# Performance work log

Measured on AMD Instinct MI355X. Metric: run time of the kernel, lower is better.

Reference implementation:

```python
import jax, jax.numpy as jnp
import numpy as np

B, N, F = 2, 2048, 64
H, C = 4, 32          # attention heads, channels per head
HID = 128             # hidden_size
HIN = H * C           # hidden_size_in = 128
MASK = -10e9          # spektral dense-GAT mask constant


def setup_inputs() -> dict:
    key = jax.random.key(0)
    ks = jax.random.split(key, 48)
    inp = {}
    inp['x'] = jax.random.normal(ks[0], (B, N, F), dtype=jnp.float32)
    adj = (jax.random.uniform(ks[1], (B, N, N)) < 0.03).astype(jnp.float32)
    inp['a'] = jnp.clip(adj + jnp.eye(N, dtype=jnp.float32)[None], 0.0, 1.0)
    inp['h_p'] = jax.random.normal(ks[2], (B, N, HID), dtype=jnp.float32) * 0.1
    inp['h_mu'] = jax.random.normal(ks[3], (B, N, HID), dtype=jnp.float32) * 0.1
    inp['h_sigma'] = jax.random.normal(ks[4], (B, N, HID), dtype=jnp.float32) * 0.1
    # GAT params
    inp['gat_kernel'] = jax.random.normal(ks[5], (F, H, C), dtype=jnp.float32) / np.float32(np.sqrt(F))
    inp['gat_attn_self'] = jax.random.normal(ks[6], (H, C), dtype=jnp.float32) * 0.1
    inp['gat_attn_neigh'] = jax.random.normal(ks[7], (H, C), dtype=jnp.float32) * 0.1
    inp['gat_bias'] = jnp.zeros((H * C,), dtype=jnp.float32)
    # GRU-style gate params for p / mu / sigma
    ki = 8
    for nm in ('p', 'mu', 'sigma'):
        for g in ('u', 'r', 'c'):
            inp[f'W_{g}_{nm}'] = jax.random.normal(ks[ki], (HID + HIN, HID), dtype=jnp.float32) / np.float32(np.sqrt(HID + HIN)); ki += 1
            inp[f'b_{g}_{nm}'] = jax.random.normal(ks[ki], (N, 1), dtype=jnp.float32) * 0.05; ki += 1
    # bilinear decoders
    for nm in ('p', 'mu', 'sigma'):
        inp[f'R_{nm}'] = jax.random.normal(ks[ki], (HID, HID), dtype=jnp.float32) / np.float32(np.sqrt(HID)); ki += 1
    return inp


def _gat(x, a, kernel, attn_self, attn_neigh, bias):
    # dense spektral GATConv, concat_heads=True, no activation
    h = jnp.einsum('bnf,fhc->bnhc', x, kernel)                 # [B,N,H,C]
    s_self = jnp.einsum('bnhc,hc->bnh', h, attn_self)          # [B,N,H]
    s_neigh = jnp.einsum('bnhc,hc->bnh', h, attn_neigh)        # [B,N,H]
    scores = s_self[:, :, None, :] + s_neigh[:, None, :, :]    # [B,N,N,H]
    scores = jax.nn.leaky_relu(scores, negative_slope=0.2)
    scores = scores + MASK * (1.0 - a)[..., None]
    attn = jax.nn.softmax(scores, axis=2)                      # softmax over neighbors j
    out = jnp.einsum('bijh,bjhc->bihc', attn, h)               # [B,N,H,C]
    return out.reshape(out.shape[0], out.shape[1], H * C) + bias


def _gru(conv, h, Wu, Wr, Wc, bu, br, bc):
    ch = jnp.concatenate([conv, h], axis=-1)                   # [B,N,HIN+HID]
    u = jax.nn.sigmoid(bu + ch @ Wu)                           # bias [N,1] broadcasts
    r = jax.nn.sigmoid(br + ch @ Wr)
    c = jnp.tanh(bc + jnp.concatenate([conv, r * h], axis=-1) @ Wc)
    return u * h + (1.0 - u) * c


def _bilinear(h, R):
    return jnp.einsum('bnh,hk,bmk->bnm', h, R, h)              # x R x^T


def reference(x, a, h_p, h_mu, h_sigma,
              gat_kernel, gat_attn_self, gat_attn_neigh, gat_bias,
              W_u_p, b_u_p, W_r_p, b_r_p, W_c_p, b_c_p,
              W_u_mu, b_u_mu, W_r_mu, b_r_mu, W_c_mu, b_c_mu,
              W_u_sigma, b_u_sigma, W_r_sigma, b_r_sigma, W_c_sigma, b_c_sigma,
              R_p, R_mu, R_sigma):
    conv = _gat(x, a, gat_kernel, gat_attn_self, gat_attn_neigh, gat_bias)
    hp = _gru(conv, h_p, W_u_p, W_r_p, W_c_p, b_u_p, b_r_p, b_c_p)
    hmu = _gru(conv, h_mu, W_u_mu, W_r_mu, W_c_mu, b_u_mu, b_r_mu, b_c_mu)
    hsg = _gru(conv, h_sigma, W_u_sigma, W_r_sigma, W_c_sigma, b_u_sigma, b_r_sigma, b_c_sigma)
    p = _bilinear(hp, R_p)
    mu = _bilinear(hmu, R_mu)
    sigma = _bilinear(hsg, R_sigma)
    logits = jnp.stack([p, mu, sigma], axis=-1)                # [B,N,N,3]
    return logits, hp, hmu, hsg
```

## Files before the change

kernel.cpp:

```cpp
#include <hip/hip_runtime.h>
#include <hip/hip_bf16.h>

typedef __attribute__((ext_vector_type(4))) float f32x4;
typedef __attribute__((ext_vector_type(8))) short bf16x8;

static constexpr int B   = 2;
static constexpr int N   = 2048;
static constexpr int F   = 64;
static constexpr int H   = 4;
static constexpr int HID = 128;
static constexpr int BN  = B * N;
static constexpr size_t LOG_SZ = (size_t)B * N * N * 3;

__device__ __forceinline__ float sigmoidf_(float x) { return 1.0f / (1.0f + __expf(-x)); }
__device__ __forceinline__ float tanhf_(float x) {
  float e = __expf(2.0f * x);
  return 1.0f - 2.0f / (e + 1.0f);
}
__device__ __forceinline__ void split_bf16(float v, short& hi, short& lo) {
  unsigned u = __float_as_uint(v);
  unsigned hr = (u + 0x7FFFu + ((u >> 16) & 1u)) >> 16;
  hi = (short)hr;
  float hv = __uint_as_float(hr << 16);
  float res = v - hv;
  unsigned u2 = __float_as_uint(res);
  lo = (short)((u2 + 0x7FFFu + ((u2 >> 16) & 1u)) >> 16);
}

__device__ __forceinline__ void stage16(const short* gp, short* lp) {
  __builtin_amdgcn_global_load_lds(
      (const __attribute__((address_space(1))) void*)gp,
      (__attribute__((address_space(3))) void*)lp, 16, 0, 0);
}

struct PreArgs {
  const float* x; const float* gk; const float* asel; const float* anei;
  float* hfeat; float* sself; float* sneigh;
  const float* h[3];
  short* hh[3]; short* hl[3];
  const float* src[12];
  short* whi[12]; short* wlo[12];
  int nks[12];
};
__global__ __launch_bounds__(256) void k_pre(PreArgs pa) {
  const int bid = blockIdx.x;
  if (bid < BN / 2) {
    const int t = threadIdx.x;
    const int r = t >> 7, tt = t & 127;
    const int bn = bid * 2 + r;
    __shared__ float xs[2][F];
    if (tt < F) xs[r][tt] = pa.x[(size_t)bn * F + tt];
    const size_t o = (size_t)bn * HID + tt;
    { short hi, lo; split_bf16(pa.h[0][o], hi, lo); pa.hh[0][o] = hi; pa.hl[0][o] = lo; }
    { short hi, lo; split_bf16(pa.h[1][o], hi, lo); pa.hh[1][o] = hi; pa.hl[1][o] = lo; }
    { short hi, lo; split_bf16(pa.h[2][o], hi, lo); pa.hh[2][o] = hi; pa.hl[2][o] = lo; }
    __syncthreads();
    float acc = 0.f;
    #pragma unroll 8
    for (int f = 0; f < F; ++f) acc += xs[r][f] * pa.gk[f * HID + tt];
    pa.hfeat[o] = acc;
    float ps = acc * pa.asel[tt];
    float pn = acc * pa.anei[tt];
    #pragma unroll
    for (int d = 16; d >= 1; d >>= 1) {
      ps += __shfl_xor(ps, d, 32);
      pn += __shfl_xor(pn, d, 32);
    }
    if ((tt & 31) == 0) {
      pa.sself [bn * H + (tt >> 5)] = ps;
      pa.sneigh[bn * H + (tt >> 5)] = pn;
    }
  } else {
    const int pb = bid - BN / 2;
    const int m = pb >> 3, cf = pb & 7;
    const int nksv = pa.nks[m];
    const int wv = threadIdx.x >> 6, lane = threadIdx.x & 63;
    const float* src = pa.src[m];
    short* ph = pa.whi[m];
    short* pl = pa.wlo[m];
    const int col = cf * 16 + (lane & 15);
    const int krow = (lane >> 4) * 8;
    for (int ks = wv; ks < nksv; ks += 4) {
      bf16x8 vh, vl;
      #pragma unroll
      for (int e = 0; e < 8; ++e) {
        const int k = ks * 32 + krow + e;
        short hi, lo; split_bf16(src[(size_t)k * HID + col], hi, lo);
        vh[e] = hi; vl[e] = lo;
      }
      const size_t o = (((size_t)cf * nksv + ks) * 64 + lane) * 8;
      *(bf16x8*)&ph[o] = vh;
      *(bf16x8*)&pl[o] = vl;
    }
  }
}

__global__ __launch_bounds__(256) void k_attn(
    const float* __restrict__ a, const float* __restrict__ hfeat,
    const float* __restrict__ sself, const float* __restrict__ sneigh,
    const float* __restrict__ bias,
    short* __restrict__ conv_hi, short* __restrict__ conv_lo) {
  const int wv   = threadIdx.x >> 6;
  const int lane = threadIdx.x & 63;
  const int bi   = blockIdx.x;
  const int bbase = bi & ~(N - 1);
  __shared__ int   nbr[4][128];
  __shared__ float wts[4][128][4];
  __shared__ float racc[4][128];
  __shared__ float rden[4][4];
  int*   nb      = nbr[wv];
  float (*wt)[4] = wts[wv];

  const float si0 = sself[bi * H + 0];
  const float si1 = sself[bi * H + 1];
  const float si2 = sself[bi * H + 2];
  const float si3 = sself[bi * H + 3];
  float den0 = 0.f, den1 = 0.f, den2 = 0.f, den3 = 0.f;
  float acc0 = 0.f, acc1 = 0.f;
  const unsigned long long lmlt = ((unsigned long long)1 << lane) - 1ull;
  const float* arow = a + (size_t)bi * N + wv * 512;
  const float* hb   = hfeat + (size_t)bbase * HID;
  const float* snb  = sneigh + (size_t)bbase * H;
  const int h0 = lane >> 5;
  const int jbase0 = wv * 512;
  int num = 0;

  auto flush = [&]() {
    asm volatile("s_waitcnt lgkmcnt(0)" ::: "memory");
    for (int n = lane; n < num; n += 64) {
      const int j = nb[n];
      f32x4 sn = *(const f32x4*)&snb[(size_t)j * H];
      float s0 = si0 + sn[0]; s0 = (s0 > 0.f) ? s0 : 0.2f * s0;
      float s1 = si1 + sn[1]; s1 = (s1 > 0.f) ? s1 : 0.2f * s1;
      float s2 = si2 + sn[2]; s2 = (s2 > 0.f) ? s2 : 0.2f * s2;
      float s3 = si3 + sn[3]; s3 = (s3 > 0.f) ? s3 : 0.2f * s3;
      float w0 = __expf(s0), w1 = __expf(s1), w2 = __expf(s2), w3 = __expf(s3);
      wt[n][0] = w0; wt[n][1] = w1; wt[n][2] = w2; wt[n][3] = w3;
      den0 += w0; den1 += w1; den2 += w2; den3 += w3;
    }
    asm volatile("s_waitcnt lgkmcnt(0)" ::: "memory");
    #pragma unroll 4
    for (int n = 0; n < num; ++n) {
      const int j  = nb[n];
      const float wA = wt[n][h0];
      const float wB = wt[n][h0 + 2];
      const float* hr = hb + (size_t)j * HID;
      acc0 += wA * hr[lane];
      acc1 += wB * hr[lane + 64];
    }
    asm volatile("s_waitcnt lgkmcnt(0)" ::: "memory");
    num = 0;
  };

  #pragma unroll
  for (int jb = 0; jb < 512; jb += 256) {
    f32x4 av = *(const f32x4*)&arow[jb + lane * 4];
    #pragma unroll
    for (int e = 0; e < 4; ++e) {
      const unsigned long long m = __ballot(av[e] > 0.5f);
      if (av[e] > 0.5f) {
        const int pos = num + __popcll(m & lmlt);
        nb[pos] = jbase0 + jb + lane * 4 + e;
      }
      num += __popcll(m);
      if (num > 64) flush();
    }
  }
  if (num > 0) flush();

  #pragma unroll
  for (int d = 32; d >= 1; d >>= 1) {
    den0 += __shfl_xor(den0, d, 64);
    den1 += __shfl_xor(den1, d, 64);
    den2 += __shfl_xor(den2, d, 64);
    den3 += __shfl_xor(den3, d, 64);
  }
  racc[wv][lane]      = acc0;
  racc[wv][lane + 64] = acc1;
  if (lane == 0) {
    rden[wv][0] = den0; rden[wv][1] = den1;
    rden[wv][2] = den2; rden[wv][3] = den3;
  }
  __syncthreads();
  if (threadIdx.x < HID) {
    const int ch = threadIdx.x;
    const float tot = racc[0][ch] + racc[1][ch] + racc[2][ch] + racc[3][ch];
    const int hh = ch >> 5;
    const float dd = rden[0][hh] + rden[1][hh] + rden[2][hh] + rden[3][hh];
    const float v = tot / dd + bias[ch];
    short hi, lo; split_bf16(v, hi, lo);
    conv_hi[(size_t)bi * HID + ch] = hi;
    conv_lo[(size_t)bi * HID + ch] = lo;
  }
}

struct GArgs {
  const short* chi; const short* clo;
  const float* h[3];
  const short* hhi[3]; const short* hlo[3];
  const float* bu[3]; const float* br[3]; const float* bc[3];
  const short* WuH[3]; const short* WuL[3];
  const short* WrH[3]; const short* WrL[3];
  const short* WcH[3]; const short* WcL[3];
  const short* RtH[3]; const short* RtL[3];
  float* u_ws[3];
  short* rhh[3]; short* rhl[3];
  short* hph[3]; short* hpl[3];
  float* hout[3]; __hip_bfloat16* hb[3]; __hip_bfloat16* gb[3];
};

__global__ __launch_bounds__(256) void k_ur(GArgs ga) {
  const int wv = threadIdx.x >> 6, lane = threadIdx.x & 63;
  const int bx = blockIdx.x, cg = blockIdx.y;
  const int gate = blockIdx.z & 1, cell = blockIdx.z >> 1;
  const int lr = lane & 15, lg = lane >> 4, kb = lg * 8;
  const int R0 = bx * 64 + wv * 16;
  __shared__ short wlds[2][16][64][8];

  bf16x8 a_h[8], a_l[8];
  {
    const size_t ab = (size_t)(R0 + lr) * HID + kb;
    const short* hhi = ga.hhi[cell]; const short* hlo = ga.hlo[cell];
    #pragma unroll
    for (int ks = 0; ks < 4; ++ks) {
      a_h[ks]     = *(const bf16x8*)&ga.chi[ab + ks * 32];
      a_l[ks]     = *(const bf16x8*)&ga.clo[ab + ks * 32];
      a_h[4 + ks] = *(const bf16x8*)&hhi[ab + ks * 32];
      a_l[4 + ks] = *(const bf16x8*)&hlo[ab + ks * 32];
    }
  }
  {
    const short* WH = gate ? ga.WrH[cell] : ga.WuH[cell];
    const short* WL = gate ? ga.WrL[cell] : ga.WuL[cell];
    #pragma unroll
    for (int i = 0; i < 8; ++i) {
      const int fid = wv * 8 + i;
      const int combo = fid >> 4, f = fid & 15;
      const short* src = combo ? WL : WH;
      const short* gp = src + (((size_t)((cg * 2 + (f >> 3)) * 8 + (f & 7))) * 64 + lane) * 8;
      stage16(gp, &wlds[combo][f][0][0]);
    }
  }
  asm volatile("s_waitcnt vmcnt(0)" ::: "memory");
  __syncthreads();

  f32x4 acc[2] = {};
  #pragma unroll
  for (int ks = 0; ks < 8; ++ks) {
    const bf16x8 ah = a_h[ks], al = a_l[ks];
    #pragma unroll
    for (int cfl = 0; cfl < 2; ++cfl) {
      const int f = cfl * 8 + ks;
      bf16x8 bh = *(const bf16x8*)&wlds[0][f][lane][0];
      bf16x8 bl = *(const bf16x8*)&wlds[1][f][lane][0];
      acc[cfl] = __builtin_amdgcn_mfma_f32_16x16x32_bf16(ah, bh, acc[cfl], 0, 0, 0);
      acc[cfl] = __builtin_amdgcn_mfma_f32_16x16x32_bf16(ah, bl, acc[cfl], 0, 0, 0);
      acc[cfl] = __builtin_amdgcn_mfma_f32_16x16x32_bf16(al, bh, acc[cfl], 0, 0, 0);
    }
  }
  if (gate == 0) {
    const float* bu = ga.bu[cell];
    float* uws = ga.u_ws[cell];
    #pragma unroll
    for (int cfl = 0; cfl < 2; ++cfl) {
      const int col = cg * 32 + cfl * 16 + lr;
      #pragma unroll
      for (int q = 0; q < 4; ++q) {
        const int row = R0 + lg * 4 + q;
        uws[(size_t)row * HID + col] = sigmoidf_(acc[cfl][q] + bu[row & (N - 1)]);
      }
    }
  } else {
    const float* br = ga.br[cell];
    const float* hsrc = ga.h[cell];
    short* rhh = ga.rhh[cell]; short* rhl = ga.rhl[cell];
    #pragma unroll
    for (int cfl = 0; cfl < 2; ++cfl) {
      const int col = cg * 32 + cfl * 16 + lr;
      #pragma unroll
      for (int q = 0; q < 4; ++q) {
        const int row = R0 + lg * 4 + q;
        const float rv = sigmoidf_(acc[cfl][q] + br[row & (N - 1)]);
        const float rhv = rv * hsrc[(size_t)row * HID + col];
        short hi, lo; split_bf16(rhv, hi, lo);
        rhh[(size_t)row * HID + col] = hi;
        rhl[(size_t)row * HID + col] = lo;
      }
    }
  }
}

__global__ __launch_bounds__(256) void k_c(GArgs ga) {
  const int wv = threadIdx.x >> 6, lane = threadIdx.x & 63;
  const int bx = blockIdx.x, cg = blockIdx.y, cell = blockIdx.z;
  const int lr = lane & 15, lg = lane >> 4, kb = lg * 8;
  const int R0 = bx * 64 + wv * 16;
  __shared__ short wlds[2][16][64][8];

  bf16x8 a_h[8], a_l[8];
  {
    const size_t ab = (size_t)(R0 + lr) * HID + kb;
    const short* rhh = ga.rhh[cell]; const short* rhl = ga.rhl[cell];
    #pragma unroll
    for (int ks = 0; ks < 4; ++ks) {
      a_h[ks]     = *(const bf16x8*)&ga.chi[ab + ks * 32];
      a_l[ks]     = *(const bf16x8*)&ga.clo[ab + ks * 32];
      a_h[4 + ks] = *(const bf16x8*)&rhh[ab + ks * 32];
      a_l[4 + ks] = *(const bf16x8*)&rhl[ab + ks * 32];
    }
  }
  {
    const short* WH = ga.WcH[cell];
    const short* WL = ga.WcL[cell];
    #pragma unroll
    for (int i = 0; i < 8; ++i) {
      const int fid = wv * 8 + i;
      const int combo = fid >> 4, f = fid & 15;
      const short* src = combo ? WL : WH;
      const short* gp = src + (((size_t)((cg * 2 + (f >> 3)) * 8 + (f & 7))) * 64 + lane) * 8;
      stage16(gp, &wlds[combo][f][0][0]);
    }
  }
  asm volatile("s_waitcnt vmcnt(0)" ::: "memory");
  __syncthreads();

  f32x4 acc[2] = {};
  #pragma unroll
  for (int ks = 0; ks < 8; ++ks) {
    const bf16x8 ah = a_h[ks], al = a_l[ks];
    #pragma unroll
    for (int cfl = 0; cfl < 2; ++cfl) {
      const int f = cfl * 8 + ks;
      bf16x8 bh = *(const bf16x8*)&wlds[0][f][lane][0];
      bf16x8 bl = *(const bf16x8*)&wlds[1][f][lane][0];
      acc[cfl] = __builtin_amdgcn_mfma_f32_16x16x32_bf16(ah, bh, acc[cfl], 0, 0, 0);
      acc[cfl] = __builtin_amdgcn_mfma_f32_16x16x32_bf16(ah, bl, acc[cfl], 0, 0, 0);
      acc[cfl] = __builtin_amdgcn_mfma_f32_16x16x32_bf16(al, bh, acc[cfl], 0, 0, 0);
    }
  }
  const float* bc = ga.bc[cell];
  const float* uw = ga.u_ws[cell];
  const float* hsrc = ga.h[cell];
  float* hout = ga.hout[cell];
  __hip_bfloat16* hbo = ga.hb[cell];
  short* hph = ga.hph[cell]; short* hpl = ga.hpl[cell];
  #pragma unroll
  for (int cfl = 0; cfl < 2; ++cfl) {
    const int col = cg * 32 + cfl * 16 + lr;
    #pragma unroll
    for (int q = 0; q < 4; ++q) {
      const int row = R0 + lg * 4 + q;
      const float cv = tanhf_(acc[cfl][q] + bc[row & (N - 1)]);
      const float uv = uw[(size_t)row * HID + col];
      const float hv = hsrc[(size_t)row * HID + col];
      const float o = uv * hv + (1.f - uv) * cv;
      __builtin_nontemporal_store(o, &hout[(size_t)row * HID + col]);
      hbo[(size_t)row * HID + col] = __float2bfloat16(o);
      short hi, lo; split_bf16(o, hi, lo);
      hph[(size_t)row * HID + col] = hi;
      hpl[(size_t)row * HID + col] = lo;
    }
  }
}

__global__ __launch_bounds__(256) void k_g(GArgs ga) {
  const int wv = threadIdx.x >> 6, lane = threadIdx.x & 63;
  const int bx = blockIdx.x, cg = blockIdx.y, cell = blockIdx.z;
  const int lr = lane & 15, lg = lane >> 4, kb = lg * 8;
  const int R0 = bx * 64 + wv * 16;
  __shared__ short wlds[2][8][64][8];

  bf16x8 a_h[4], a_l[4];
  {
    const size_t ab = (size_t)(R0 + lr) * HID + kb;
    const short* hph = ga.hph[cell]; const short* hpl = ga.hpl[cell];
    #pragma unroll
    for (int ks = 0; ks < 4; ++ks) {
      a_h[ks] = *(const bf16x8*)&hph[ab + ks * 32];
      a_l[ks] = *(const bf16x8*)&hpl[ab + ks * 32];
    }
  }
  {
    #pragma unroll
    for (int i = 0; i < 4; ++i) {
      const int fid = wv * 4 + i;
      const int combo = fid >> 3, f = fid & 7;
      const short* src = combo ? ga.RtL[cell] : ga.RtH[cell];
      const short* gp = src + (((size_t)((cg * 2 + (f >> 2)) * 4 + (f & 3))) * 64 + lane) * 8;
      stage16(gp, &wlds[combo][f][0][0]);
    }
  }
  asm volatile("s_waitcnt vmcnt(0)" ::: "memory");
  __syncthreads();

  f32x4 acc[2] = {};
  #pragma unroll
  for (int ks = 0; ks < 4; ++ks) {
    const bf16x8 ah = a_h[ks], al = a_l[ks];
    #pragma unroll
    for (int cfl = 0; cfl < 2; ++cfl) {
      const int f = cfl * 4 + ks;
      bf16x8 bh = *(const bf16x8*)&wlds[0][f][lane][0];
      bf16x8 bl = *(const bf16x8*)&wlds[1][f][lane][0];
      acc[cfl] = __builtin_amdgcn_mfma_f32_16x16x32_bf16(ah, bh, acc[cfl], 0, 0, 0);
      acc[cfl] = __builtin_amdgcn_mfma_f32_16x16x32_bf16(ah, bl, acc[cfl], 0, 0, 0);
      acc[cfl] = __builtin_amdgcn_mfma_f32_16x16x32_bf16(al, bh, acc[cfl], 0, 0, 0);
    }
  }
  __hip_bfloat16* gbo = ga.gb[cell];
  #pragma unroll
  for (int cfl = 0; cfl < 2; ++cfl) {
    const int col = cg * 32 + cfl * 16 + lr;
    #pragma unroll
    for (int q = 0; q < 4; ++q) {
      const int row = R0 + lg * 4 + q;
      gbo[(size_t)row * HID + col] = __float2bfloat16(acc[cfl][q]);
    }
  }
}

__global__ __launch_bounds__(256) void k_bilinear(
    const __hip_bfloat16* __restrict__ g0, const __hip_bfloat16* __restrict__ g1,
    const __hip_bfloat16* __restrict__ g2, const __hip_bfloat16* __restrict__ h0,
    const __hip_bfloat16* __restrict__ h1, const __hip_bfloat16* __restrict__ h2,
    float* __restrict__ out) {
  const int ti = blockIdx.x, tj = blockIdx.y, b = blockIdx.z;
  const int t = threadIdx.x;
  const int w = t >> 6, l = t & 63;
  const int wi = w >> 1, wj = w & 1;
  const int i_base = ti * 64 + wi * 32;
  const int j_base = tj * 64 + wj * 32;
  const __hip_bfloat16* gbs[3] = {g0, g1, g2};
  const __hip_bfloat16* hbs[3] = {h0, h1, h2};
  const int lr = l & 15;
  const int kb = (l >> 4) * 8;
  f32x4 acc[3][2][2] = {};
  for (int k0 = 0; k0 < HID; k0 += 32) {
    bf16x8 af[3][2], bfr[3][2];
    #pragma unroll
    for (int d = 0; d < 3; ++d) {
      #pragma unroll
      for (int m = 0; m < 2; ++m) {
        af[d][m]  = *(const bf16x8*)&gbs[d][(size_t)(b * N + i_base + m * 16 + lr) * HID + k0 + kb];
        bfr[d][m] = *(const bf16x8*)&hbs[d][(size_t)(b * N + j_base + m * 16 + lr) * HID + k0 + kb];
      }
    }
    #pragma unroll
    for (int d = 0; d < 3; ++d)
      #pragma unroll
      for (int mi = 0; mi < 2; ++mi)
        #pragma unroll
        for (int mj = 0; mj < 2; ++mj)
          acc[d][mi][mj] = __builtin_amdgcn_mfma_f32_16x16x32_bf16(
              af[d][mi], bfr[d][mj], acc[d][mi][mj], 0, 0, 0);
  }
  const int orow = (l >> 4) * 4;
  const int col  = l & 15;
  #pragma unroll
  for (int mi = 0; mi < 2; ++mi)
    #pragma unroll
    for (int mj = 0; mj < 2; ++mj)
      #pragma unroll
      for (int r = 0; r < 4; ++r) {
        const int row = i_base + mi * 16 + orow + r;
        const int cc  = j_base + mj * 16 + col;
        float* p = &out[(((size_t)(b * N + row)) * N + cc) * 3];
        __builtin_nontemporal_store(acc[0][mi][mj][r], p + 0);
        __builtin_nontemporal_store(acc[1][mi][mj][r], p + 1);
        __builtin_nontemporal_store(acc[2][mi][mj][r], p + 2);
      }
}

extern "C" void kernel_launch(void* const* d_in, const int* in_sizes, int n_in,
                              void* d_out, int out_size, void* d_ws, size_t ws_size,
                              hipStream_t stream) {
  (void)in_sizes; (void)n_in; (void)out_size; (void)ws_size;
  const float* a    = (const float*)d_in[1];
  const float* bias = (const float*)d_in[8];

  float* ws      = (float*)d_ws;
  float* hfeat   = ws;
  float* sself   = hfeat + (size_t)BN * HID;
  float* sneigh  = sself + (size_t)BN * H;
  float* u_ws0   = sneigh + (size_t)BN * H;
  short* sp      = (short*)(u_ws0 + 3 * (size_t)BN * HID);
  auto alloc_s = [&](size_t n) { short* p = sp; sp += n; return p; };

  short* conv_hi = alloc_s((size_t)BN * HID);
  short* conv_lo = alloc_s((size_t)BN * HID);
  short* h_hi[3]; short* h_lo[3];
  for (int c = 0; c < 3; ++c) { h_hi[c] = alloc_s((size_t)BN * HID); h_lo[c] = alloc_s((size_t)BN * HID); }
  short* rh_hi[3]; short* rh_lo[3];
  for (int c = 0; c < 3; ++c) { rh_hi[c] = alloc_s((size_t)BN * HID); rh_lo[c] = alloc_s((size_t)BN * HID); }
  short* hp_hi[3]; short* hp_lo[3];
  for (int c = 0; c < 3; ++c) { hp_hi[c] = alloc_s((size_t)BN * HID); hp_lo[c] = alloc_s((size_t)BN * HID); }
  __hip_bfloat16* hbb[3]; __hip_bfloat16* gbb[3];
  for (int c = 0; c < 3; ++c) {
    hbb[c] = (__hip_bfloat16*)alloc_s((size_t)BN * HID);
    gbb[c] = (__hip_bfloat16*)alloc_s((size_t)BN * HID);
  }

  float* out = (float*)d_out;

  PreArgs pa;
  pa.x = (const float*)d_in[0];
  pa.gk = (const float*)d_in[5];
  pa.asel = (const float*)d_in[6];
  pa.anei = (const float*)d_in[7];
  pa.hfeat = hfeat; pa.sself = sself; pa.sneigh = sneigh;

  GArgs ga;
  ga.chi = conv_hi; ga.clo = conv_lo;
  ga.h[0] = (const float*)d_in[2];
  ga.h[1] = (const float*)d_in[3];
  ga.h[2] = (const float*)d_in[4];
  for (int c = 0; c < 3; ++c) {
    pa.h[c] = ga.h[c];
    pa.hh[c] = h_hi[c]; pa.hl[c] = h_lo[c];
    const int base = 9 + c * 6;
    ga.hhi[c] = h_hi[c]; ga.hlo[c] = h_lo[c];
    ga.bu[c] = (const float*)d_in[base + 1];
    ga.br[c] = (const float*)d_in[base + 3];
    ga.bc[c] = (const float*)d_in[base + 5];
    short* wu_h = alloc_s(256 * 128); short* wu_l = alloc_s(256 * 128);
    short* wr_h = alloc_s(256 * 128); short* wr_l = alloc_s(256 * 128);
    short* wc_h = alloc_s(256 * 128); short* wc_l = alloc_s(256 * 128);
    short* rt_h = alloc_s(128 * 128); short* rt_l = alloc_s(128 * 128);
    const int pb = c * 4;
    pa.src[pb + 0] = (const float*)d_in[base + 0]; pa.whi[pb + 0] = wu_h; pa.wlo[pb + 0] = wu_l; pa.nks[pb + 0] = 8;
    pa.src[pb + 1] = (const float*)d_in[base + 2]; pa.whi[pb + 1] = wr_h; pa.wlo[pb + 1] = wr_l; pa.nks[pb + 1] = 8;
    pa.src[pb + 2] = (const float*)d_in[base + 4]; pa.whi[pb + 2] = wc_h; pa.wlo[pb + 2] = wc_l; pa.nks[pb + 2] = 8;
    pa.src[pb + 3] = (const float*)d_in[27 + c];   pa.whi[pb + 3] = rt_h; pa.wlo[pb + 3] = rt_l; pa.nks[pb + 3] = 4;
    ga.WuH[c] = wu_h; ga.WuL[c] = wu_l;
    ga.WrH[c] = wr_h; ga.WrL[c] = wr_l;
    ga.WcH[c] = wc_h; ga.WcL[c] = wc_l;
    ga.RtH[c] = rt_h; ga.RtL[c] = rt_l;
    ga.u_ws[c] = u_ws0 + (size_t)c * BN * HID;
    ga.rhh[c] = rh_hi[c]; ga.rhl[c] = rh_lo[c];
    ga.hph[c] = hp_hi[c]; ga.hpl[c] = hp_lo[c];
    ga.hout[c] = out + LOG_SZ + (size_t)c * BN * HID;
    ga.hb[c] = hbb[c];
    ga.gb[c] = gbb[c];
  }

  k_pre<<<BN / 2 + 96, 256, 0, stream>>>(pa);
  k_attn<<<BN, 256, 0, stream>>>(a, hfeat, sself, sneigh, bias, conv_hi, conv_lo);
  k_ur<<<dim3(BN / 64, 4, 6), 256, 0, stream>>>(ga);
  k_c<<<dim3(BN / 64, 4, 3), 256, 0, stream>>>(ga);
  k_g<<<dim3(BN / 64, 4, 3), 256, 0, stream>>>(ga);
  dim3 g2(N / 64, N / 64, B);
  k_bilinear<<<g2, 256, 0, stream>>>(gbb[0], gbb[1], gbb[2],
                                     hbb[0], hbb[1], hbb[2], out);
}
```

Baseline: 115.3 us.

## Fuse update and reset gates in one kernel; enlarge bilinear tiles with swizzled order

The u and r gate GEMMs now run in the same block, so the A-operand fragments (conv and h, hi/lo splits) are loaded once and reused for both gates, and the grid z-dimension halves. The bilinear kernel moves to 512-thread blocks covering 128 rows of the output tile and remaps block ids with a grouped swizzle to improve L2 reuse of the g/h operands. In exchange, k_ur uses twice the LDS and more accumulator registers, and there are fewer blocks in flight.

```diff
diff --git a/kernel.cpp b/kernel.cpp
--- a/kernel.cpp
+++ b/kernel.cpp
@@ -211,11 +211,10 @@
 
 __global__ __launch_bounds__(256) void k_ur(GArgs ga) {
   const int wv = threadIdx.x >> 6, lane = threadIdx.x & 63;
-  const int bx = blockIdx.x, cg = blockIdx.y;
-  const int gate = blockIdx.z & 1, cell = blockIdx.z >> 1;
+  const int bx = blockIdx.x, cg = blockIdx.y, cell = blockIdx.z;
   const int lr = lane & 15, lg = lane >> 4, kb = lg * 8;
   const int R0 = bx * 64 + wv * 16;
-  __shared__ short wlds[2][16][64][8];
+  __shared__ short wlds[4][16][64][8];
 
   bf16x8 a_h[8], a_l[8];
   {
@@ -230,62 +229,54 @@
     }
   }
   {
-    const short* WH = gate ? ga.WrH[cell] : ga.WuH[cell];
-    const short* WL = gate ? ga.WrL[cell] : ga.WuL[cell];
-    #pragma unroll
-    for (int i = 0; i < 8; ++i) {
-      const int fid = wv * 8 + i;
-      const int combo = fid >> 4, f = fid & 15;
-      const short* src = combo ? WL : WH;
-      const short* gp = src + (((size_t)((cg * 2 + (f >> 3)) * 8 + (f & 7))) * 64 + lane) * 8;
-      stage16(gp, &wlds[combo][f][0][0]);
+    const short* srcs[4] = { ga.WuH[cell], ga.WuL[cell], ga.WrH[cell], ga.WrL[cell] };
+    const short* sp = srcs[wv];
+    #pragma unroll
+    for (int f = 0; f < 16; ++f) {
+      const short* gp = sp + (((size_t)((cg * 2 + (f >> 3)) * 8 + (f & 7))) * 64 + lane) * 8;
+      stage16(gp, &wlds[wv][f][0][0]);
     }
   }
   asm volatile("s_waitcnt vmcnt(0)" ::: "memory");
   __syncthreads();
 
-  f32x4 acc[2] = {};
+  f32x4 au[2] = {}, ar[2] = {};
   #pragma unroll
   for (int ks = 0; ks < 8; ++ks) {
     const bf16x8 ah = a_h[ks], al = a_l[ks];
     #pragma unroll
     for (int cfl = 0; cfl < 2; ++cfl) {
       const int f = cfl * 8 + ks;
-      bf16x8 bh = *(const bf16x8*)&wlds[0][f][lane][0];
-      bf16x8 bl = *(const bf16x8*)&wlds[1][f][lane][0];
-      acc[cfl] = __builtin_amdgcn_mfma_f32_16x16x32_bf16(ah, bh, acc[cfl], 0, 0, 0);
-      acc[cfl] = __builtin_amdgcn_mfma_f32_16x16x32_bf16(ah, bl, acc[cfl], 0, 0, 0);
-      acc[cfl] = __builtin_amdgcn_mfma_f32_16x16x32_bf16(al, bh, acc[cfl], 0, 0, 0);
-    }
-  }
-  if (gate == 0) {
-    const float* bu = ga.bu[cell];
-    float* uws = ga.u_ws[cell];
-    #pragma unroll
-    for (int cfl = 0; cfl < 2; ++cfl) {
-      const int col = cg * 32 + cfl * 16 + lr;
-      #pragma unroll
-      for (int q = 0; q < 4; ++q) {
-        const int row = R0 + lg * 4 + q;
-        uws[(size_t)row * HID + col] = sigmoidf_(acc[cfl][q] + bu[row & (N - 1)]);
-      }
-    }
-  } else {
-    const float* br = ga.br[cell];
-    const float* hsrc = ga.h[cell];
-    short* rhh = ga.rhh[cell]; short* rhl = ga.rhl[cell];
-    #pragma unroll
-    for (int cfl = 0; cfl < 2; ++cfl) {
-      const int col = cg * 32 + cfl * 16 + lr;
-      #pragma unroll
-      for (int q = 0; q < 4; ++q) {
-        const int row = R0 + lg * 4 + q;
-        const float rv = sigmoidf_(acc[cfl][q] + br[row & (N - 1)]);
-        const float rhv = rv * hsrc[(size_t)row * HID + col];
-        short hi, lo; split_bf16(rhv, hi, lo);
-        rhh[(size_t)row * HID + col] = hi;
-        rhl[(size_t)row * HID + col] = lo;
-      }
+      bf16x8 buh = *(const bf16x8*)&wlds[0][f][lane][0];
+      bf16x8 bul = *(const bf16x8*)&wlds[1][f][lane][0];
+      bf16x8 brh = *(const bf16x8*)&wlds[2][f][lane][0];
+      bf16x8 brl = *(const bf16x8*)&wlds[3][f][lane][0];
+      au[cfl] = __builtin_amdgcn_mfma_f32_16x16x32_bf16(ah, buh, au[cfl], 0, 0, 0);
+      au[cfl] = __builtin_amdgcn_mfma_f32_16x16x32_bf16(ah, bul, au[cfl], 0, 0, 0);
+      au[cfl] = __builtin_amdgcn_mfma_f32_16x16x32_bf16(al, buh, au[cfl], 0, 0, 0);
+      ar[cfl] = __builtin_amdgcn_mfma_f32_16x16x32_bf16(ah, brh, ar[cfl], 0, 0, 0);
+      ar[cfl] = __builtin_amdgcn_mfma_f32_16x16x32_bf16(ah, brl, ar[cfl], 0, 0, 0);
+      ar[cfl] = __builtin_amdgcn_mfma_f32_16x16x32_bf16(al, brh, ar[cfl], 0, 0, 0);
+    }
+  }
+  const float* bu = ga.bu[cell];
+  const float* br = ga.br[cell];
+  const float* hsrc = ga.h[cell];
+  float* uws = ga.u_ws[cell];
+  short* rhh = ga.rhh[cell]; short* rhl = ga.rhl[cell];
+  #pragma unroll
+  for (int cfl = 0; cfl < 2; ++cfl) {
+    const int col = cg * 32 + cfl * 16 + lr;
+    #pragma unroll
+    for (int q = 0; q < 4; ++q) {
+      const int row = R0 + lg * 4 + q;
+      const int n = row & (N - 1);
+      uws[(size_t)row * HID + col] = sigmoidf_(au[cfl][q] + bu[n]);
+      const float rv = sigmoidf_(ar[cfl][q] + br[n]);
+      const float rhv = rv * hsrc[(size_t)row * HID + col];
+      short hi, lo; split_bf16(rhv, hi, lo);
+      rhh[(size_t)row * HID + col] = hi;
+      rhl[(size_t)row * HID + col] = lo;
     }
   }
 }
@@ -419,16 +410,19 @@
   }
 }
 
-__global__ __launch_bounds__(256) void k_bilinear(
+__global__ __launch_bounds__(512) void k_bilinear(
     const __hip_bfloat16* __restrict__ g0, const __hip_bfloat16* __restrict__ g1,
     const __hip_bfloat16* __restrict__ g2, const __hip_bfloat16* __restrict__ h0,
     const __hip_bfloat16* __restrict__ h1, const __hip_bfloat16* __restrict__ h2,
     float* __restrict__ out) {
-  const int ti = blockIdx.x, tj = blockIdx.y, b = blockIdx.z;
+  const int id  = blockIdx.y * 16 + blockIdx.x;
+  const int id2 = (id & 7) * 64 + (id >> 3);
+  const int ti = id2 & 15, tj = id2 >> 4;
+  const int b = blockIdx.z;
   const int t = threadIdx.x;
   const int w = t >> 6, l = t & 63;
   const int wi = w >> 1, wj = w & 1;
-  const int i_base = ti * 64 + wi * 32;
+  const int i_base = ti * 128 + wi * 32;
   const int j_base = tj * 64 + wj * 32;
   const __hip_bfloat16* gbs[3] = {g0, g1, g2};
   const __hip_bfloat16* hbs[3] = {h0, h1, h2};
@@ -545,10 +539,10 @@
 
   k_pre<<<BN / 2 + 96, 256, 0, stream>>>(pa);
   k_attn<<<BN, 256, 0, stream>>>(a, hfeat, sself, sneigh, bias, conv_hi, conv_lo);
-  k_ur<<<dim3(BN / 64, 4, 6), 256, 0, stream>>>(ga);
+  k_ur<<<dim3(BN / 64, 4, 3), 256, 0, stream>>>(ga);
   k_c<<<dim3(BN / 64, 4, 3), 256, 0, stream>>>(ga);
   k_g<<<dim3(BN / 64, 4, 3), 256, 0, stream>>>(ga);
-  dim3 g2(N / 64, N / 64, B);
-  k_bilinear<<<g2, 256, 0, stream>>>(gbb[0], gbb[1], gbb[2],
+  dim3 g2(N / 128, N / 64, B);
+  k_bilinear<<<g2, 512, 0, stream>>>(gbb[0], gbb[1], gbb[2],
                                      hbb[0], hbb[1], hbb[2], out);
 }
```

Result: no change. 116.8 us (+1.3%).
